# Kernel optimization log

Hardware: AMD Instinct MI355X
Metric: run time of the kernel (lower is better)

## Reference

```python
import jax, jax.numpy as jnp
import numpy as np
from jax import lax

COUNT_NORM_FACTOR = 0.1


def setup_inputs() -> dict:
    key = jax.random.key(0)
    ks = jax.random.split(key, 8)
    B, NA, NT, D = 4096, 16, 16, 128
    task_embeds = jax.random.normal(ks[0], (B, NT, D), dtype=jnp.float32)
    task_nonag_counts = jax.random.uniform(ks[1], (B, NT), dtype=jnp.float32)
    agent_embeds = jax.random.normal(ks[2], (B, NA, D), dtype=jnp.float32)
    task_mask = jnp.zeros((B, NT), dtype=bool)
    agent_mask = jnp.zeros((B, NA), dtype=jnp.float32)  # 0 = active agent
    u = jax.random.uniform(ks[3], (NA, B, NT), dtype=jnp.float32,
                           minval=1e-6, maxval=1.0 - 1e-6)
    gumbels = -jnp.log(-jnp.log(u))
    W_count = jax.random.normal(ks[4], (2, D), dtype=jnp.float32) / np.sqrt(2.0)
    b_count = jnp.zeros((D,), dtype=jnp.float32)
    W_upd = jax.random.normal(ks[5], (2 * D, D), dtype=jnp.float32) / np.sqrt(2.0 * D)
    b_upd = jnp.zeros((D,), dtype=jnp.float32)
    return dict(task_embeds=task_embeds, task_nonag_counts=task_nonag_counts,
                agent_embeds=agent_embeds, task_mask=task_mask,
                agent_mask=agent_mask, gumbels=gumbels,
                W_count=W_count, b_count=b_count, W_upd=W_upd, b_upd=b_upd)


def _autoreg(task_embeds, task_nonag_counts, agent_embeds, task_mask,
             agent_mask, gumbels, W_count, b_count, W_upd, b_upd):
    B, NT, D = task_embeds.shape
    scale = jnp.sqrt(jnp.asarray(D, task_embeds.dtype))
    neg_min = jnp.finfo(task_embeds.dtype).min

    def step(carry, xs):
        te, counts = carry  # te: [B,NT,D], counts: [B,NT]
        ag_emb, g, amask = xs  # [B,D], [B,NT], [B]
        # count embedding: Linear(2, D) on stack([nonag, ag], -1)
        cnt_in = jnp.stack([task_nonag_counts, counts], axis=-1)  # [B,NT,2]
        cnt_e = cnt_in @ W_count + b_count  # [B,NT,D]
        # pointer logits
        logits = jnp.einsum('bd,btd->bt', ag_emb, te + cnt_e) / scale
        masked = jnp.where(task_mask, neg_min, logits)
        # RelaxedOneHotCategorical(temp=1).rsample via gumbel-softmax
        soft = jax.nn.softmax(masked + g, axis=-1)
        onehot = jax.nn.one_hot(jnp.argmax(soft, axis=-1), NT, dtype=soft.dtype)
        hard = onehot - lax.stop_gradient(soft) + soft
        agm = (1.0 - amask)[:, None]  # [B,1]
        hard = hard * agm
        hstop = lax.stop_gradient(hard)
        counts = counts + hstop * COUNT_NORM_FACTOR
        # embedding update: Linear(2D, D) on relu(concat([te, agent_embed]))
        upd_in = jnp.concatenate(
            [te, jnp.broadcast_to(ag_emb[:, None, :], (B, NT, D))], axis=-1)
        upd = jax.nn.relu(upd_in) @ W_upd + b_upd  # [B,NT,D]
        te = te + upd * hstop[..., None] * agm[..., None]
        return (te, counts), hard

    init = (task_embeds, jnp.zeros((B, NT), task_embeds.dtype))
    xs = (jnp.swapaxes(agent_embeds, 0, 1), gumbels, jnp.swapaxes(agent_mask, 0, 1))
    _, allocs = lax.scan(step, init, xs)  # [NA,B,NT]
    return jnp.swapaxes(allocs, 0, 1)  # [B,NA,NT]


def reference(task_embeds, task_nonag_counts, agent_embeds, task_mask,
              agent_mask, gumbels, W_count, b_count, W_upd, b_upd):
    return _autoreg(task_embeds, task_nonag_counts, agent_embeds, task_mask,
                    agent_mask, gumbels, W_count, b_count, W_upd, b_upd)
```

## Files before the change

kernel.cpp:

```cpp
#include <hip/hip_runtime.h>
#include <float.h>
#include <math.h>

#define NBATCH   4096
#define NAGENT   16
#define NTASK    16
#define DDIM     128
#define G        8
#define NTHREADS 512
#define SSEG     20

template<int CTRL>
__device__ __forceinline__ float dppf(float x) {
    return __int_as_float(__builtin_amdgcn_update_dpp(
        0, __float_as_int(x), CTRL, 0xF, 0xF, true));
}
template<int CTRL>
__device__ __forceinline__ int dppi(int x) {
    return __builtin_amdgcn_update_dpp(0, x, CTRL, 0xF, 0xF, true);
}

__global__ __launch_bounds__(NTHREADS, 2)
void alloc_policy_kernel(const float* __restrict__ task_embeds,
                         const float* __restrict__ task_nonag,
                         const float* __restrict__ agent_embeds,
                         const unsigned char* __restrict__ task_mask,
                         const float* __restrict__ agent_mask,
                         const float* __restrict__ gumbels,
                         const float* __restrict__ W_count,
                         const float* __restrict__ b_count,
                         const float* __restrict__ W_upd,
                         const float* __restrict__ b_upd,
                         float* __restrict__ out)
{
    __shared__ __align__(16) float te[G][NTASK][DDIM];
    __shared__ __align__(16) float scr[G][16 * SSEG];
    __shared__ __align__(16) float4 sdots4[G][NAGENT];
    __shared__ __align__(16) float4 upd4[G];

    const int tid  = threadIdx.x;
    const int lane = tid & 63;
    const int w    = tid >> 6;
    const int b0   = blockIdx.x * G;
    const int gb_w = b0 + w;

    const bool h0 = (lane & 1) != 0;
    const bool h1 = (lane & 2) != 0;
    const bool h2 = (lane & 4) != 0;
    const bool h3 = (lane & 8) != 0;

    const int cg   = tid >> 4;
    const int iseg = tid & 15;
    const float bu = b_upd[cg * 4 + (tid & 3)];

    const float scalef = sqrtf(128.0f);

    float4 Wq[16];
    #pragma unroll
    for (int c = 0; c < 4; ++c)
        #pragma unroll
        for (int di = 0; di < 4; ++di)
            Wq[c * 4 + di] = *(const float4*)(W_upd +
                (size_t)(iseg * 16 + c * 4 + di) * DDIM + cg * 4);

    {
        const float4* src = (const float4*)(task_embeds + (size_t)b0 * NTASK * DDIM);
        float4* dst = (float4*)(&te[0][0][0]);
        #pragma unroll
        for (int k = 0; k < (G * NTASK * DDIM / 4) / NTHREADS; ++k)
            dst[k * NTHREADS + tid] = src[k * NTHREADS + tid];
    }

    {
        const int p = tid >> 2, q = tid & 3;
        const int g = p >> 4,  a = p & 15;
        const float* agp = agent_embeds + ((size_t)(b0 + g) * NAGENT + a) * DDIM + q * 32;
        float a0 = 0.f, a1 = 0.f, a2 = 0.f;
        #pragma unroll
        for (int c = 0; c < 8; ++c) {
            const float4 av = *(const float4*)(agp + c * 4);
            const float4 w0 = *(const float4*)(W_count + q * 32 + c * 4);
            const float4 w1 = *(const float4*)(W_count + DDIM + q * 32 + c * 4);
            const float4 bc = *(const float4*)(b_count + q * 32 + c * 4);
            a0 = fmaf(av.x, w0.x, a0); a0 = fmaf(av.y, w0.y, a0);
            a0 = fmaf(av.z, w0.z, a0); a0 = fmaf(av.w, w0.w, a0);
            a1 = fmaf(av.x, w1.x, a1); a1 = fmaf(av.y, w1.y, a1);
            a1 = fmaf(av.z, w1.z, a1); a1 = fmaf(av.w, w1.w, a1);
            a2 = fmaf(av.x, bc.x, a2); a2 = fmaf(av.y, bc.y, a2);
            a2 = fmaf(av.z, bc.z, a2); a2 = fmaf(av.w, bc.w, a2);
        }
        a0 += __shfl_xor(a0, 1); a0 += __shfl_xor(a0, 2);
        a1 += __shfl_xor(a1, 1); a1 += __shfl_xor(a1, 2);
        a2 += __shfl_xor(a2, 1); a2 += __shfl_xor(a2, 2);
        if (q == 0) sdots4[g][a] = make_float4(a0, a1, a2, 0.f);
    }

    const int tau = lane & 15;
    const float nn_my = task_nonag[gb_w * NTASK + tau];
    const unsigned char mask_my = task_mask[gb_w * NTASK + tau];
    float cc_my = 0.0f;

    const float* agbase = agent_embeds + (size_t)gb_w * NAGENT * DDIM;
    float2 ag2 = *(const float2*)(agbase + lane * 2);
    float  gum = gumbels[(size_t)gb_w * NTASK + tau];
    float  amk = agent_mask[(size_t)gb_w * NAGENT + 0];

    __syncthreads();

    for (int a = 0; a < NAGENT; ++a) {
        float v[16];
        #pragma unroll
        for (int t = 0; t < 16; ++t) {
            const float2 t2 = *(const float2*)(&te[w][t][lane * 2]);
            v[t] = fmaf(ag2.y, t2.y, ag2.x * t2.x);
        }
        float p8[8];
        #pragma unroll
        for (int m2 = 0; m2 < 8; ++m2) {
            const float lo = v[2 * m2], hi = v[2 * m2 + 1];
            const float send = h0 ? lo : hi;
            const float mine = h0 ? hi : lo;
            p8[m2] = mine + dppf<0xB1>(send);
        }
        float p4[4];
        #pragma unroll
        for (int m2 = 0; m2 < 4; ++m2) {
            const float lo = p8[2 * m2], hi = p8[2 * m2 + 1];
            const float send = h1 ? lo : hi;
            const float mine = h1 ? hi : lo;
            p4[m2] = mine + dppf<0x4E>(send);
        }
        float p2v[2];
        #pragma unroll
        for (int m2 = 0; m2 < 2; ++m2) {
            const float lo = p4[2 * m2], hi = p4[2 * m2 + 1];
            const float send = h2 ? lo : hi;
            const float mine = h2 ? hi : lo;
            p2v[m2] = mine + __shfl_xor(send, 4);
        }
        float p1;
        {
            const float lo = p2v[0], hi = p2v[1];
            const float send = h3 ? lo : hi;
            const float mine = h3 ? hi : lo;
            p1 = mine + __shfl_xor(send, 8);
        }
        p1 += __shfl_xor(p1, 16);
        p1 += __shfl_xor(p1, 32);

        const float4 sd = sdots4[w][a];
        const float dot_total = p1 + fmaf(nn_my, sd.x, fmaf(cc_my, sd.y, sd.z));
        float z = dot_total / scalef;
        if (mask_my) z = -FLT_MAX;
        z = z + gum;

        float mz = z;
        mz = fmaxf(mz, dppf<0xB1>(mz));
        mz = fmaxf(mz, dppf<0x4E>(mz));
        mz = fmaxf(mz, __shfl_xor(mz, 4));
        mz = fmaxf(mz, __shfl_xor(mz, 8));
        const float e = expf(z - mz);
        float ss = e;
        ss += dppf<0xB1>(ss);
        ss += dppf<0x4E>(ss);
        ss += __shfl_xor(ss, 4);
        ss += __shfl_xor(ss, 8);
        const float sft = e / ss;

        float mx = sft;
        mx = fmaxf(mx, dppf<0xB1>(mx));
        mx = fmaxf(mx, dppf<0x4E>(mx));
        mx = fmaxf(mx, __shfl_xor(mx, 4));
        mx = fmaxf(mx, __shfl_xor(mx, 8));
        int cand = (sft == mx) ? tau : NTASK;
        cand = min(cand, dppi<0xB1>(cand));
        cand = min(cand, dppi<0x4E>(cand));
        cand = min(cand, __shfl_xor(cand, 4));
        cand = min(cand, __shfl_xor(cand, 8));
        const int bi = cand;

        const float agm = 1.0f - amk;
        const float onehot = (tau == bi) ? 1.0f : 0.0f;
        const float hh = ((onehot - sft) + sft) * agm;

        if (lane < 16)
            out[((size_t)gb_w * NAGENT + a) * NTASK + tau] = hh;
        cc_my = cc_my + hh * 0.1f;
        if (lane < 16 && tau == bi)
            upd4[w] = make_float4(__int_as_float(bi), hh, agm, 0.f);

        {
            const float2 tsel = *(const float2*)(&te[w][bi][lane * 2]);
            float2 r0, r1;
            r0.x = fmaxf(tsel.x, 0.f); r0.y = fmaxf(tsel.y, 0.f);
            r1.x = fmaxf(ag2.x, 0.f);  r1.y = fmaxf(ag2.y, 0.f);
            const int i0 = 2 * lane;
            const int i1 = 128 + 2 * lane;
            *(float2*)(&scr[w][(i0 >> 4) * SSEG + (i0 & 15)]) = r0;
            *(float2*)(&scr[w][(i1 >> 4) * SSEG + (i1 & 15)]) = r1;
        }
        __syncthreads();

        const int an = (a + 1) & 15;
        const float2 ag2n = *(const float2*)(agbase + (size_t)an * DDIM + lane * 2);
        const float  gumn = gumbels[((size_t)an * NBATCH + gb_w) * NTASK + tau];
        const float  amkn = agent_mask[(size_t)gb_w * NAGENT + an];

        float acc[32];
        #pragma unroll
        for (int j = 0; j < 32; ++j) acc[j] = 0.f;
        #pragma unroll
        for (int c = 0; c < 4; ++c) {
            const int sb = iseg * SSEG + c * 4;
            #pragma unroll
            for (int g = 0; g < 8; ++g) {
                const float4 in4 = *(const float4*)(&scr[g][sb]);
                {
                    const float4 wv = Wq[c * 4 + 0];
                    acc[g*4+0] = fmaf(in4.x, wv.x, acc[g*4+0]);
                    acc[g*4+1] = fmaf(in4.x, wv.y, acc[g*4+1]);
                    acc[g*4+2] = fmaf(in4.x, wv.z, acc[g*4+2]);
                    acc[g*4+3] = fmaf(in4.x, wv.w, acc[g*4+3]);
                }
                {
                    const float4 wv = Wq[c * 4 + 1];
                    acc[g*4+0] = fmaf(in4.y, wv.x, acc[g*4+0]);
                    acc[g*4+1] = fmaf(in4.y, wv.y, acc[g*4+1]);
                    acc[g*4+2] = fmaf(in4.y, wv.z, acc[g*4+2]);
                    acc[g*4+3] = fmaf(in4.y, wv.w, acc[g*4+3]);
                }
                {
                    const float4 wv = Wq[c * 4 + 2];
                    acc[g*4+0] = fmaf(in4.z, wv.x, acc[g*4+0]);
                    acc[g*4+1] = fmaf(in4.z, wv.y, acc[g*4+1]);
                    acc[g*4+2] = fmaf(in4.z, wv.z, acc[g*4+2]);
                    acc[g*4+3] = fmaf(in4.z, wv.w, acc[g*4+3]);
                }
                {
                    const float4 wv = Wq[c * 4 + 3];
                    acc[g*4+0] = fmaf(in4.w, wv.x, acc[g*4+0]);
                    acc[g*4+1] = fmaf(in4.w, wv.y, acc[g*4+1]);
                    acc[g*4+2] = fmaf(in4.w, wv.z, acc[g*4+2]);
                    acc[g*4+3] = fmaf(in4.w, wv.w, acc[g*4+3]);
                }
            }
        }
        float q16[16];
        #pragma unroll
        for (int m2 = 0; m2 < 16; ++m2) {
            const float lo = acc[2 * m2], hi = acc[2 * m2 + 1];
            const float send = h0 ? lo : hi;
            const float mine = h0 ? hi : lo;
            q16[m2] = mine + dppf<0xB1>(send);
        }
        float q8[8];
        #pragma unroll
        for (int m2 = 0; m2 < 8; ++m2) {
            const float lo = q16[2 * m2], hi = q16[2 * m2 + 1];
            const float send = h1 ? lo : hi;
            const float mine = h1 ? hi : lo;
            q8[m2] = mine + dppf<0x4E>(send);
        }
        float q4[4];
        #pragma unroll
        for (int m2 = 0; m2 < 4; ++m2) {
            const float lo = q8[2 * m2], hi = q8[2 * m2 + 1];
            const float send = h2 ? lo : hi;
            const float mine = h2 ? hi : lo;
            q4[m2] = mine + __shfl_xor(send, 4);
        }
        float q2[2];
        #pragma unroll
        for (int m2 = 0; m2 < 2; ++m2) {
            const float lo = q4[2 * m2], hi = q4[2 * m2 + 1];
            const float send = h3 ? lo : hi;
            const float mine = h3 ? hi : lo;
            q2[m2] = mine + __shfl_xor(send, 8);
        }
        #pragma unroll
        for (int hgi = 0; hgi < 2; ++hgi) {
            const int g = ((lane & 15) >> 2) + hgi * 4;
            const float4 u4 = upd4[g];
            const int ts = __float_as_int(u4.x);
            const float u = q2[hgi] + bu;
            const float addv = (u * u4.y) * u4.z;
            te[g][ts][cg * 4 + (tid & 3)] += addv;
        }
        __syncthreads();

        ag2 = ag2n; gum = gumn; amk = amkn;
    }
}

extern "C" void kernel_launch(void* const* d_in, const int* in_sizes, int n_in,
                              void* d_out, int out_size, void* d_ws, size_t ws_size,
                              hipStream_t stream) {
    const float*         task_embeds  = (const float*)d_in[0];
    const float*         task_nonag   = (const float*)d_in[1];
    const float*         agent_embeds = (const float*)d_in[2];
    const unsigned char* task_mask    = (const unsigned char*)d_in[3];
    const float*         agent_mask   = (const float*)d_in[4];
    const float*         gumbels      = (const float*)d_in[5];
    const float*         W_count      = (const float*)d_in[6];
    const float*         b_count      = (const float*)d_in[7];
    const float*         W_upd        = (const float*)d_in[8];
    const float*         b_upd        = (const float*)d_in[9];
    float* out = (float*)d_out;

    dim3 grid(NBATCH / G);
    dim3 block(NTHREADS);
    hipLaunchKernelGGL(alloc_policy_kernel, grid, block, 0, stream,
                       task_embeds, task_nonag, agent_embeds, task_mask,
                       agent_mask, gumbels, W_count, b_count, W_upd, b_upd, out);
}
```

Measured before the change: 125.8 us.

## Precompute next agent's pointer dots before barrier, patch updated row, use packed FMA

```diff
diff --git a/kernel.cpp b/kernel.cpp
--- a/kernel.cpp
+++ b/kernel.cpp
@@ -10,6 +10,8 @@
 #define NTHREADS 512
 #define SSEG     20
 
+typedef float f32x2 __attribute__((ext_vector_type(2)));
+
 template<int CTRL>
 __device__ __forceinline__ float dppf(float x) {
     return __int_as_float(__builtin_amdgcn_update_dpp(
@@ -18,6 +20,16 @@
 template<int CTRL>
 __device__ __forceinline__ int dppi(int x) {
     return __builtin_amdgcn_update_dpp(0, x, CTRL, 0xF, 0xF, true);
+}
+
+template<int SEL>
+__device__ __forceinline__ void pk_fma_b(f32x2& acc, f32x2 a, f32x2 b) {
+    if constexpr (SEL == 0)
+        asm("v_pk_fma_f32 %0, %1, %2, %0 op_sel:[0,0,0] op_sel_hi:[0,1,1]"
+            : "+v"(acc) : "v"(a), "v"(b));
+    else
+        asm("v_pk_fma_f32 %0, %1, %2, %0 op_sel:[1,0,0] op_sel_hi:[1,1,1]"
+            : "+v"(acc) : "v"(a), "v"(b));
 }
 
 __global__ __launch_bounds__(NTHREADS, 2)
@@ -55,13 +67,16 @@
 
     const float scalef = sqrtf(128.0f);
 
-    float4 Wq[16];
+    f32x2 W01[16], W23[16];
     #pragma unroll
     for (int c = 0; c < 4; ++c)
         #pragma unroll
-        for (int di = 0; di < 4; ++di)
-            Wq[c * 4 + di] = *(const float4*)(W_upd +
+        for (int di = 0; di < 4; ++di) {
+            const float4 wv = *(const float4*)(W_upd +
                 (size_t)(iseg * 16 + c * 4 + di) * DDIM + cg * 4);
+            W01[c * 4 + di] = f32x2{wv.x, wv.y};
+            W23[c * 4 + di] = f32x2{wv.z, wv.w};
+        }
 
     {
         const float4* src = (const float4*)(task_embeds + (size_t)b0 * NTASK * DDIM);
@@ -105,14 +120,12 @@
     float  gum = gumbels[(size_t)gb_w * NTASK + tau];
     float  amk = agent_mask[(size_t)gb_w * NAGENT + 0];
 
-    __syncthreads();
-
-    for (int a = 0; a < NAGENT; ++a) {
+    auto wave_dots = [&](float2 agv) -> float {
         float v[16];
         #pragma unroll
         for (int t = 0; t < 16; ++t) {
             const float2 t2 = *(const float2*)(&te[w][t][lane * 2]);
-            v[t] = fmaf(ag2.y, t2.y, ag2.x * t2.x);
+            v[t] = fmaf(agv.y, t2.y, agv.x * t2.x);
         }
         float p8[8];
         #pragma unroll
@@ -147,9 +160,16 @@
         }
         p1 += __shfl_xor(p1, 16);
         p1 += __shfl_xor(p1, 32);
-
+        return p1;
+    };
+
+    __syncthreads();
+
+    float p1_cur = wave_dots(ag2);
+
+    for (int a = 0; a < NAGENT; ++a) {
         const float4 sd = sdots4[w][a];
-        const float dot_total = p1 + fmaf(nn_my, sd.x, fmaf(cc_my, sd.y, sd.z));
+        const float dot_total = p1_cur + fmaf(nn_my, sd.x, fmaf(cc_my, sd.y, sd.z));
         float z = dot_total / scalef;
         if (mask_my) z = -FLT_MAX;
         z = z + gum;
@@ -199,56 +219,40 @@
             *(float2*)(&scr[w][(i0 >> 4) * SSEG + (i0 & 15)]) = r0;
             *(float2*)(&scr[w][(i1 >> 4) * SSEG + (i1 & 15)]) = r1;
         }
-        __syncthreads();
 
         const int an = (a + 1) & 15;
         const float2 ag2n = *(const float2*)(agbase + (size_t)an * DDIM + lane * 2);
         const float  gumn = gumbels[((size_t)an * NBATCH + gb_w) * NTASK + tau];
         const float  amkn = agent_mask[(size_t)gb_w * NAGENT + an];
 
-        float acc[32];
-        #pragma unroll
-        for (int j = 0; j < 32; ++j) acc[j] = 0.f;
+        __syncthreads();
+
+        f32x2 acc01[G], acc23[G];
+        #pragma unroll
+        for (int g = 0; g < G; ++g) { acc01[g] = f32x2{0.f, 0.f}; acc23[g] = f32x2{0.f, 0.f}; }
         #pragma unroll
         for (int c = 0; c < 4; ++c) {
             const int sb = iseg * SSEG + c * 4;
             #pragma unroll
             for (int g = 0; g < 8; ++g) {
                 const float4 in4 = *(const float4*)(&scr[g][sb]);
-                {
-                    const float4 wv = Wq[c * 4 + 0];
-                    acc[g*4+0] = fmaf(in4.x, wv.x, acc[g*4+0]);
-                    acc[g*4+1] = fmaf(in4.x, wv.y, acc[g*4+1]);
-                    acc[g*4+2] = fmaf(in4.x, wv.z, acc[g*4+2]);
-                    acc[g*4+3] = fmaf(in4.x, wv.w, acc[g*4+3]);
-                }
-                {
-                    const float4 wv = Wq[c * 4 + 1];
-                    acc[g*4+0] = fmaf(in4.y, wv.x, acc[g*4+0]);
-                    acc[g*4+1] = fmaf(in4.y, wv.y, acc[g*4+1]);
-                    acc[g*4+2] = fmaf(in4.y, wv.z, acc[g*4+2]);
-                    acc[g*4+3] = fmaf(in4.y, wv.w, acc[g*4+3]);
-                }
-                {
-                    const float4 wv = Wq[c * 4 + 2];
-                    acc[g*4+0] = fmaf(in4.z, wv.x, acc[g*4+0]);
-                    acc[g*4+1] = fmaf(in4.z, wv.y, acc[g*4+1]);
-                    acc[g*4+2] = fmaf(in4.z, wv.z, acc[g*4+2]);
-                    acc[g*4+3] = fmaf(in4.z, wv.w, acc[g*4+3]);
-                }
-                {
-                    const float4 wv = Wq[c * 4 + 3];
-                    acc[g*4+0] = fmaf(in4.w, wv.x, acc[g*4+0]);
-                    acc[g*4+1] = fmaf(in4.w, wv.y, acc[g*4+1]);
-                    acc[g*4+2] = fmaf(in4.w, wv.z, acc[g*4+2]);
-                    acc[g*4+3] = fmaf(in4.w, wv.w, acc[g*4+3]);
-                }
+                const f32x2 ixy = f32x2{in4.x, in4.y};
+                const f32x2 izw = f32x2{in4.z, in4.w};
+                pk_fma_b<0>(acc01[g], ixy, W01[c * 4 + 0]);
+                pk_fma_b<1>(acc01[g], ixy, W01[c * 4 + 1]);
+                pk_fma_b<0>(acc01[g], izw, W01[c * 4 + 2]);
+                pk_fma_b<1>(acc01[g], izw, W01[c * 4 + 3]);
+                pk_fma_b<0>(acc23[g], ixy, W23[c * 4 + 0]);
+                pk_fma_b<1>(acc23[g], ixy, W23[c * 4 + 1]);
+                pk_fma_b<0>(acc23[g], izw, W23[c * 4 + 2]);
+                pk_fma_b<1>(acc23[g], izw, W23[c * 4 + 3]);
             }
         }
         float q16[16];
         #pragma unroll
         for (int m2 = 0; m2 < 16; ++m2) {
-            const float lo = acc[2 * m2], hi = acc[2 * m2 + 1];
+            const float lo = (m2 & 1) ? acc23[m2 >> 1].x : acc01[m2 >> 1].x;
+            const float hi = (m2 & 1) ? acc23[m2 >> 1].y : acc01[m2 >> 1].y;
             const float send = h0 ? lo : hi;
             const float mine = h0 ? hi : lo;
             q16[m2] = mine + dppf<0xB1>(send);
@@ -277,6 +281,10 @@
             const float mine = h3 ? hi : lo;
             q2[m2] = mine + __shfl_xor(send, 8);
         }
+
+        float p1n = 0.f;
+        if (a < NAGENT - 1) p1n = wave_dots(make_float2(ag2n.x, ag2n.y));
+
         #pragma unroll
         for (int hgi = 0; hgi < 2; ++hgi) {
             const int g = ((lane & 15) >> 2) + hgi * 4;
@@ -287,6 +295,18 @@
             te[g][ts][cg * 4 + (tid & 3)] += addv;
         }
         __syncthreads();
+
+        if (a < NAGENT - 1) {
+            const float2 tn = *(const float2*)(&te[w][bi][lane * 2]);
+            float pr = fmaf(ag2n.y, tn.y, ag2n.x * tn.x);
+            pr += dppf<0xB1>(pr);
+            pr += dppf<0x4E>(pr);
+            pr += __shfl_xor(pr, 4);
+            pr += __shfl_xor(pr, 8);
+            pr += __shfl_xor(pr, 16);
+            pr += __shfl_xor(pr, 32);
+            p1_cur = (tau == bi) ? pr : p1n;
+        }
 
         ag2 = ag2n; gum = gumn; amk = amkn;
     }
```

After: 131.2 us. 4.2% more time.
